# Kernel tuning notes

Measured on AMD Instinct MI355X. Metric: run time of the kernel, lower is better.

Reference implementation:

```python
import jax, jax.numpy as jnp
import numpy as np

D_MODEL = 2048
N_Q = 16
N_KV = 4
HEAD_DIM = 128
WINDOW = 512
ROPE_BASE = 10000.0


def _rope_cos_sin(T, dtype):
    half = HEAD_DIM // 2
    inv_freq = 1.0 / (ROPE_BASE ** (jnp.arange(0, half, dtype=jnp.float32) * 2.0 / HEAD_DIM))
    pos = jnp.arange(T, dtype=jnp.float32)
    ang = pos[:, None] * inv_freq[None, :]            # [T, half]
    emb = jnp.concatenate([ang, ang], axis=-1)        # [T, HEAD_DIM]
    return jnp.cos(emb).astype(dtype), jnp.sin(emb).astype(dtype)


def _rotate_half(x):
    x1, x2 = jnp.split(x, 2, axis=-1)
    return jnp.concatenate([-x2, x1], axis=-1)


def _apply_rope(t, cos, sin):
    # t: [B, H, T, hd]; cos/sin: [T, hd]
    return t * cos[None, None, :, :] + _rotate_half(t) * sin[None, None, :, :]


def setup_inputs() -> dict:
    key = jax.random.key(0)
    ks = jax.random.split(key, 5)
    s = 0.02
    return {
        "x": jax.random.normal(ks[0], (2, 2048, D_MODEL), dtype=jnp.float32),
        "wq": jax.random.normal(ks[1], (D_MODEL, N_Q * HEAD_DIM), dtype=jnp.float32) * s,
        "wk": jax.random.normal(ks[2], (D_MODEL, N_KV * HEAD_DIM), dtype=jnp.float32) * s,
        "wv": jax.random.normal(ks[3], (D_MODEL, N_KV * HEAD_DIM), dtype=jnp.float32) * s,
        "wo": jax.random.normal(ks[4], (N_Q * HEAD_DIM, D_MODEL), dtype=jnp.float32) * s,
    }


def reference(x, wq, wk, wv, wo):
    B, T, _ = x.shape
    q = (x @ wq).reshape(B, T, N_Q, HEAD_DIM).transpose(0, 2, 1, 3)    # [B,Hq,T,hd]
    k = (x @ wk).reshape(B, T, N_KV, HEAD_DIM).transpose(0, 2, 1, 3)   # [B,Hkv,T,hd]
    v = (x @ wv).reshape(B, T, N_KV, HEAD_DIM).transpose(0, 2, 1, 3)

    cos, sin = _rope_cos_sin(T, x.dtype)
    q = _apply_rope(q, cos, sin)
    k = _apply_rope(k, cos, sin)

    # GQA: repeat_interleave kv heads to match q heads
    g = N_Q // N_KV
    k = jnp.repeat(k, g, axis=1)
    v = jnp.repeat(v, g, axis=1)

    scale = 1.0 / np.sqrt(HEAD_DIM)
    scores = jnp.einsum("bhqd,bhkd->bhqk", q, k) * scale

    idx = jnp.arange(T)
    diff = idx[:, None] - idx[None, :]
    keep = (diff >= 0) & (diff < WINDOW)               # causal & sliding window
    scores = jnp.where(keep[None, None, :, :], scores, jnp.finfo(scores.dtype).min)
    attn = jax.nn.softmax(scores, axis=-1)

    out = jnp.einsum("bhqk,bhkd->bhqd", attn, v)       # [B,Hq,T,hd]
    out = out.transpose(0, 2, 1, 3).reshape(B, T, N_Q * HEAD_DIM)
    return out @ wo
```

## Files before the change

### kernel.cpp

```cpp
#include <hip/hip_runtime.h>

#define T_SEQ   2048
#define DM      2048
#define N_Q     16
#define N_KV    4
#define HD      128
#define WIN     512
#define NB      2
#define NQKV    3072
#define QK_SCALE 0.08838834764831845f

typedef short bf16x8 __attribute__((ext_vector_type(8)));
typedef float f32x4  __attribute__((ext_vector_type(4)));

__device__ __forceinline__ unsigned short f2bf(float f) {
    union { float f; unsigned u; } v; v.f = f;
    unsigned u = v.u;
    u += 0x7fffu + ((u >> 16) & 1u);
    return (unsigned short)(u >> 16);
}
__device__ __forceinline__ float bf2f(unsigned short h) {
    union { unsigned u; float f; } v; v.u = ((unsigned)h) << 16;
    return v.f;
}

#define GLOAD_LDS16(g, l) __builtin_amdgcn_global_load_lds( \
    (const __attribute__((address_space(1))) void*)(g),     \
    (__attribute__((address_space(3))) void*)(l), 16, 0, 0)


struct us4 { unsigned short a, b, c, d; };

__global__ __launch_bounds__(256)
void f32_to_bf16_vec(const float* __restrict__ in, unsigned short* __restrict__ out, long n) {
    long i = ((long)blockIdx.x * 256 + threadIdx.x) * 4;
    if (i < n) {
        float4 f = *(const float4*)(in + i);
        us4 o; o.a = f2bf(f.x); o.b = f2bf(f.y); o.c = f2bf(f.z); o.d = f2bf(f.w);
        *(us4*)(out + i) = o;
    }
}

__global__ __launch_bounds__(256)
void transpose_w(const float* __restrict__ in, unsigned short* __restrict__ out, int R, int C) {
    __shared__ float tile[32][33];
    const int c0 = blockIdx.x * 32, r0 = blockIdx.y * 32;
    const int tx = threadIdx.x, ty = threadIdx.y;
#pragma unroll
    for (int i = 0; i < 4; ++i)
        tile[ty + i * 8][tx] = in[(long)(r0 + ty + i * 8) * C + c0 + tx];
    __syncthreads();
#pragma unroll
    for (int i = 0; i < 4; ++i)
        out[(long)(c0 + ty + i * 8) * R + r0 + tx] = f2bf(tile[tx][ty + i * 8]);
}

__global__ __launch_bounds__(256)
void rope_table(float* __restrict__ cosT, float* __restrict__ sinT) {
    const int idx = blockIdx.x * 256 + threadIdx.x;
    const int t = idx >> 6, d = idx & 63;
    const float inv = __expf(-(float)d * (9.210340371976184f / 64.0f));
    const float ang = (float)t * inv;
    cosT[idx] = cosf(ang);
    sinT[idx] = sinf(ang);
}

__global__ __launch_bounds__(256)
void rope_apply(unsigned short* __restrict__ qkv,
                const float* __restrict__ cosT, const float* __restrict__ sinT) {
    const int idx = blockIdx.x * 256 + threadIdx.x;
    const int d = idx & 63;
    const int hh = (idx >> 6) % 20;
    const int row = idx / (64 * 20);
    const int t = row & (T_SEQ - 1);
    const int col = (hh < N_Q) ? hh * HD + d : DM + (hh - N_Q) * HD + d;
    unsigned short* p = qkv + (long)row * NQKV + col;
    const float a = bf2f(p[0]), b = bf2f(p[64]);
    const float c = cosT[t * 64 + d], s = sinT[t * 64 + d];
    float o1 = a * c - b * s;
    float o2 = b * c + a * s;
    if (hh < N_Q) { o1 *= QK_SCALE; o2 *= QK_SCALE; }
    p[0]  = f2bf(o1);
    p[64] = f2bf(o2);
}

__global__ __launch_bounds__(256)
void transpose_v(const unsigned short* __restrict__ qkv, unsigned short* __restrict__ vt) {
    __shared__ unsigned short tile[32][33];
    const int bh = blockIdx.z;
    const int d0 = blockIdx.y * 32;
    const int t0 = blockIdx.x * 32;
    const int tx = threadIdx.x, ty = threadIdx.y;
    const long inbase = (long)(bh >> 2) * T_SEQ;
    const int coff = DM + N_KV * HD + (bh & 3) * HD;
#pragma unroll
    for (int i = 0; i < 4; ++i)
        tile[ty + i * 8][tx] = qkv[(inbase + t0 + ty + i * 8) * NQKV + coff + d0 + tx];
    __syncthreads();
#pragma unroll
    for (int i = 0; i < 4; ++i)
        vt[((long)bh * HD + d0 + ty + i * 8) * T_SEQ + t0 + tx] = tile[tx][ty + i * 8];
}


template<int OUT_BF16>
__global__ __launch_bounds__(256)
void gemm_bt(const unsigned short* __restrict__ A,
             const unsigned short* __restrict__ Bt,
             void* __restrict__ Cvoid, int K, int ldc) {
    __shared__ __align__(16) unsigned short sA[128 * 64];
    __shared__ __align__(16) unsigned short sB[128 * 64];
    const int tid = threadIdx.x;
    const int lane = tid & 63;
    const int wid = tid >> 6;
    const int wr = (wid >> 1) * 64, wc = (wid & 1) * 64;
    const long Arow0 = (long)blockIdx.y * 128;
    const long Brow0 = (long)blockIdx.x * 128;

    f32x4 acc[4][4] = {};

    for (int kt = 0; kt < K; kt += 64) {
        __syncthreads();
#pragma unroll
        for (int n = 0; n < 4; ++n) {
            const int linb = n * 256 + wid * 64;
            const int lin  = linb + lane;
            const int row  = lin >> 3;
            const int sc   = (lin & 7) ^ (row & 7);
            const unsigned short* gA = A  + (Arow0 + row) * K + kt + sc * 8;
            const unsigned short* gB = Bt + (Brow0 + row) * K + kt + sc * 8;
            GLOAD_LDS16(gA, &sA[linb * 8]);
            GLOAD_LDS16(gB, &sB[linb * 8]);
        }
        __syncthreads();
#pragma unroll
        for (int kk = 0; kk < 2; ++kk) {
            bf16x8 av[4], bv[4];
#pragma unroll
            for (int i = 0; i < 4; ++i) {
                const int row = wr + i * 16 + (lane & 15);
                const int c = (kk * 4 + (lane >> 4)) ^ (row & 7);
                av[i] = *(const bf16x8*)&sA[row * 64 + c * 8];
            }
#pragma unroll
            for (int j = 0; j < 4; ++j) {
                const int row = wc + j * 16 + (lane & 15);
                const int c = (kk * 4 + (lane >> 4)) ^ (row & 7);
                bv[j] = *(const bf16x8*)&sB[row * 64 + c * 8];
            }
#pragma unroll
            for (int i = 0; i < 4; ++i)
#pragma unroll
                for (int j = 0; j < 4; ++j)
                    acc[i][j] = __builtin_amdgcn_mfma_f32_16x16x32_bf16(av[i], bv[j], acc[i][j], 0, 0, 0);
        }
    }

    const int r0 = (int)Arow0 + wr + ((lane >> 4) << 2);
    const int c0 = (int)Brow0 + wc + (lane & 15);
    if (OUT_BF16) {
        unsigned short* C = (unsigned short*)Cvoid;
#pragma unroll
        for (int i = 0; i < 4; ++i)
#pragma unroll
            for (int j = 0; j < 4; ++j)
#pragma unroll
                for (int r = 0; r < 4; ++r)
                    C[(long)(r0 + i * 16 + r) * ldc + c0 + j * 16] = f2bf(acc[i][j][r]);
    } else {
        float* C = (float*)Cvoid;
#pragma unroll
        for (int i = 0; i < 4; ++i)
#pragma unroll
            for (int j = 0; j < 4; ++j)
#pragma unroll
                for (int r = 0; r < 4; ++r)
                    C[(long)(r0 + i * 16 + r) * ldc + c0 + j * 16] = acc[i][j][r];
    }
}


__global__ __launch_bounds__(256)
void attn_kernel(const unsigned short* __restrict__ qkv,
                 const unsigned short* __restrict__ vt,
                 unsigned short* __restrict__ aout) {
    const int qt = blockIdx.x, h = blockIdx.y, b = blockIdx.z;
    const int tid = threadIdx.x, lane = tid & 63, w = tid >> 6;
    const int q0w = qt * 64 + w * 16;
    const int hkv = h >> 2;
    const int lo = lane & 15, hi = lane >> 4;

    __shared__ __align__(16) unsigned short sK[64 * 128];
    __shared__ __align__(16) unsigned short sV[128 * 64];
    __shared__ __align__(16) unsigned short plds[4][16 * 64];
    unsigned short* pl = plds[w];

    bf16x8 qf[4];
    {
        const unsigned short* qp = qkv + (long)(b * T_SEQ + q0w + lo) * NQKV + h * HD + hi * 8;
#pragma unroll
        for (int s = 0; s < 4; ++s) qf[s] = *(const bf16x8*)(qp + s * 32);
    }

    f32x4 of[8] = {};
    float m_r[4] = { -1e30f, -1e30f, -1e30f, -1e30f };
    float s_r[4] = { 0.f, 0.f, 0.f, 0.f };

    int kstart = qt * 64 - (WIN - 1);
    if (kstart < 0) kstart = 0;
    kstart &= ~63;
    const int kend = qt * 64 + 63;

    const unsigned short* kbase = qkv + (long)b * T_SEQ * NQKV + DM + hkv * HD;
    const unsigned short* vbase = vt + (long)(b * N_KV + hkv) * HD * T_SEQ;

    int krow[4], kck[4], vrow[4], vck[4];
#pragma unroll
    for (int u = 0; u < 4; ++u) {
        const int i = w * 4 + u;
        krow[u] = i * 4 + (lane >> 4);
        kck[u]  = (lane & 15) ^ (krow[u] & 7);
        vrow[u] = i * 8 + (lane >> 3);
        vck[u]  = (lane & 7) ^ (vrow[u] & 7);
    }

    for (int kt = kstart; kt <= kend; kt += 64) {
        __syncthreads();
#pragma unroll
        for (int u = 0; u < 4; ++u) {
            const int i = w * 4 + u;
            GLOAD_LDS16(kbase + (long)(kt + krow[u]) * NQKV + kck[u] * 8, &sK[i * 512]);
            GLOAD_LDS16(vbase + (long)vrow[u] * T_SEQ + kt + vck[u] * 8, &sV[i * 512]);
        }
        __syncthreads();

        f32x4 sf[4] = {};
        __builtin_amdgcn_s_setprio(1);
#pragma unroll
        for (int n = 0; n < 4; ++n) {
            const int row = n * 16 + lo;
#pragma unroll
            for (int s = 0; s < 4; ++s) {
                const int c = (s * 4 + hi) ^ (row & 7);
                bf16x8 kf = *(const bf16x8*)&sK[row * 128 + c * 8];
                sf[n] = __builtin_amdgcn_mfma_f32_16x16x32_bf16(qf[s], kf, sf[n], 0, 0, 0);
            }
        }
        __builtin_amdgcn_s_setprio(0);

        float pf[4][4];
#pragma unroll
        for (int r = 0; r < 4; ++r) {
            const int q = q0w + hi * 4 + r;
            float sv[4];
#pragma unroll
            for (int n = 0; n < 4; ++n) {
                const int d = q - (kt + n * 16 + lo);
                sv[n] = (d >= 0 && d < WIN) ? sf[n][r] : -1e30f;
            }
            float mx = fmaxf(fmaxf(sv[0], sv[1]), fmaxf(sv[2], sv[3]));
#pragma unroll
            for (int off = 1; off < 16; off <<= 1) mx = fmaxf(mx, __shfl_xor(mx, off));
            const float mnew = fmaxf(m_r[r], mx);
            const float resc = __expf(m_r[r] - mnew);
            float ps = 0.f;
#pragma unroll
            for (int n = 0; n < 4; ++n) { pf[n][r] = __expf(sv[n] - mnew); ps += pf[n][r]; }
#pragma unroll
            for (int off = 1; off < 16; off <<= 1) ps += __shfl_xor(ps, off);
            s_r[r] = s_r[r] * resc + ps;
            m_r[r] = mnew;
#pragma unroll
            for (int j = 0; j < 8; ++j) of[j][r] *= resc;
        }

#pragma unroll
        for (int n = 0; n < 4; ++n)
#pragma unroll
            for (int r = 0; r < 4; ++r) {
                const int row = hi * 4 + r;
                const int key = n * 16 + lo;
                const int sw = ((key >> 3) ^ (row & 7)) * 8 + (key & 7);
                pl[row * 64 + sw] = f2bf(pf[n][r]);
            }
        asm volatile("s_waitcnt lgkmcnt(0)" ::: "memory");
        __builtin_amdgcn_sched_barrier(0);
        bf16x8 pa[2];
#pragma unroll
        for (int ks = 0; ks < 2; ++ks) {
            const int c = (ks * 4 + hi) ^ (lo & 7);
            pa[ks] = *(const bf16x8*)&pl[lo * 64 + c * 8];
        }

        __builtin_amdgcn_s_setprio(1);
#pragma unroll
        for (int j = 0; j < 8; ++j) {
            const int row = j * 16 + lo;
#pragma unroll
            for (int ks = 0; ks < 2; ++ks) {
                const int c = (ks * 4 + hi) ^ (row & 7);
                bf16x8 vf = *(const bf16x8*)&sV[row * 64 + c * 8];
                of[j] = __builtin_amdgcn_mfma_f32_16x16x32_bf16(pa[ks], vf, of[j], 0, 0, 0);
            }
        }
        __builtin_amdgcn_s_setprio(0);
    }

#pragma unroll
    for (int r = 0; r < 4; ++r) {
        const int q = q0w + hi * 4 + r;
        const float inv = 1.0f / s_r[r];
        unsigned short* op = aout + (long)(b * T_SEQ + q) * DM + h * HD + lo;
#pragma unroll
        for (int j = 0; j < 8; ++j) op[j * 16] = f2bf(of[j][r] * inv);
    }
}


extern "C" void kernel_launch(void* const* d_in, const int* in_sizes, int n_in,
                              void* d_out, int out_size, void* d_ws, size_t ws_size,
                              hipStream_t stream) {
    (void)in_sizes; (void)n_in; (void)out_size; (void)ws_size;
    const float* x  = (const float*)d_in[0];
    const float* wq = (const float*)d_in[1];
    const float* wk = (const float*)d_in[2];
    const float* wv = (const float*)d_in[3];
    const float* wo = (const float*)d_in[4];
    float* out = (float*)d_out;
    char* ws = (char*)d_ws;

    unsigned short* xbf   = (unsigned short*)(ws);
    unsigned short* wqkvT = (unsigned short*)(ws + 16777216);
    unsigned short* woT   = (unsigned short*)(ws + 29360128);
    unsigned short* qkv   = (unsigned short*)(ws + 37748736);
    unsigned short* vt    = (unsigned short*)(ws + 62914560);
    unsigned short* aout  = (unsigned short*)(ws + 67108864);
    float* cosT = (float*)(ws + 83886080);
    float* sinT = (float*)(ws + 84410368);

    const long Mx = (long)NB * T_SEQ * DM;
    f32_to_bf16_vec<<<dim3(8192), dim3(256), 0, stream>>>(x, xbf, Mx);
    transpose_w<<<dim3(64, 64), dim3(32, 8), 0, stream>>>(wq, wqkvT, DM, DM);
    transpose_w<<<dim3(16, 64), dim3(32, 8), 0, stream>>>(wk, wqkvT + (long)DM * DM, DM, 512);
    transpose_w<<<dim3(16, 64), dim3(32, 8), 0, stream>>>(wv, wqkvT + (long)(DM + 512) * DM, DM, 512);
    transpose_w<<<dim3(64, 64), dim3(32, 8), 0, stream>>>(wo, woT, DM, DM);
    rope_table<<<dim3(512), dim3(256), 0, stream>>>(cosT, sinT);

    gemm_bt<1><<<dim3(NQKV / 128, 32), dim3(256), 0, stream>>>(xbf, wqkvT, qkv, DM, NQKV);
    rope_apply<<<dim3(20480), dim3(256), 0, stream>>>(qkv, cosT, sinT);
    transpose_v<<<dim3(64, 4, 8), dim3(32, 8), 0, stream>>>(qkv, vt);
    attn_kernel<<<dim3(32, 16, 2), dim3(256), 0, stream>>>(qkv, vt, aout);
    gemm_bt<0><<<dim3(DM / 128, 32), dim3(256), 0, stream>>>(aout, woT, out, DM, DM);
}
```

Measured before the change: 198.6 us.

## Double-buffer attention K/V tiles, transpose score MFMA, lazy softmax rescale, swizzle GEMM grid

The attention kernel now double-buffers K and V tiles in LDS, prefetching the next tile while computing the current one. It swaps the MFMA operands so each lane holds one query row, which cuts the row-max and sum reductions to two shuffles. It folds log2(e) into the Q scale so exp2 can be used, and skips the output rescale unless the max grows by more than 8. The GEMM also remaps block indices across 8 groups for better cache locality, and P is packed to bf16 with a single instruction. In exchange the kernel uses twice the LDS for K/V, which may lower occupancy.

```diff
diff --git a/kernel.cpp b/kernel.cpp
--- a/kernel.cpp
+++ b/kernel.cpp
@@ -8,7 +8,7 @@
 #define WIN     512
 #define NB      2
 #define NQKV    3072
-#define QK_SCALE 0.08838834764831845f
+#define QK_SCALE_L2E 0.12751744f
 
 typedef short bf16x8 __attribute__((ext_vector_type(8)));
 typedef float f32x4  __attribute__((ext_vector_type(4)));
@@ -22,6 +22,11 @@
 __device__ __forceinline__ float bf2f(unsigned short h) {
     union { unsigned u; float f; } v; v.u = ((unsigned)h) << 16;
     return v.f;
+}
+__device__ __forceinline__ unsigned cvt_pk_bf16(float a, float b) {
+    unsigned r;
+    asm("v_cvt_pk_bf16_f32 %0, %1, %2" : "=v"(r) : "v"(a), "v"(b));
+    return r;
 }
 
 #define GLOAD_LDS16(g, l) __builtin_amdgcn_global_load_lds( \
@@ -79,7 +84,7 @@
     const float c = cosT[t * 64 + d], s = sinT[t * 64 + d];
     float o1 = a * c - b * s;
     float o2 = b * c + a * s;
-    if (hh < N_Q) { o1 *= QK_SCALE; o2 *= QK_SCALE; }
+    if (hh < N_Q) { o1 *= QK_SCALE_L2E; o2 *= QK_SCALE_L2E; }
     p[0]  = f2bf(o1);
     p[64] = f2bf(o2);
 }
@@ -114,8 +119,13 @@
     const int lane = tid & 63;
     const int wid = tid >> 6;
     const int wr = (wid >> 1) * 64, wc = (wid & 1) * 64;
-    const long Arow0 = (long)blockIdx.y * 128;
-    const long Brow0 = (long)blockIdx.x * 128;
+
+    const int gx = gridDim.x;
+    const int nwg = gx * gridDim.y;
+    int flat = blockIdx.y * gx + blockIdx.x;
+    flat = (flat & 7) * (nwg >> 3) + (flat >> 3);
+    const long Arow0 = (long)(flat / gx) * 128;
+    const long Brow0 = (long)(flat % gx) * 128;
 
     f32x4 acc[4][4] = {};
 
@@ -190,8 +200,8 @@
     const int hkv = h >> 2;
     const int lo = lane & 15, hi = lane >> 4;
 
-    __shared__ __align__(16) unsigned short sK[64 * 128];
-    __shared__ __align__(16) unsigned short sV[128 * 64];
+    __shared__ __align__(16) unsigned short sK[2][64 * 128];
+    __shared__ __align__(16) unsigned short sV[2][128 * 64];
     __shared__ __align__(16) unsigned short plds[4][16 * 64];
     unsigned short* pl = plds[w];
 
@@ -203,8 +213,8 @@
     }
 
     f32x4 of[8] = {};
-    float m_r[4] = { -1e30f, -1e30f, -1e30f, -1e30f };
-    float s_r[4] = { 0.f, 0.f, 0.f, 0.f };
+    float m_r = -1e30f;
+    float s_r = 0.f;
 
     int kstart = qt * 64 - (WIN - 1);
     if (kstart < 0) kstart = 0;
@@ -224,15 +234,21 @@
         vck[u]  = (lane & 7) ^ (vrow[u] & 7);
     }
 
+#define STAGE(bf, kt_) do {                                                          \
+    _Pragma("unroll")                                                                \
+    for (int u = 0; u < 4; ++u) {                                                    \
+        const int i = w * 4 + u;                                                     \
+        GLOAD_LDS16(kbase + (long)((kt_) + krow[u]) * NQKV + kck[u] * 8, &sK[bf][i * 512]); \
+        GLOAD_LDS16(vbase + (long)vrow[u] * T_SEQ + (kt_) + vck[u] * 8, &sV[bf][i * 512]);  \
+    } } while (0)
+
+    STAGE(0, kstart);
+    asm volatile("s_waitcnt vmcnt(0)" ::: "memory");
+    __syncthreads();
+
+    int buf = 0;
     for (int kt = kstart; kt <= kend; kt += 64) {
-        __syncthreads();
-#pragma unroll
-        for (int u = 0; u < 4; ++u) {
-            const int i = w * 4 + u;
-            GLOAD_LDS16(kbase + (long)(kt + krow[u]) * NQKV + kck[u] * 8, &sK[i * 512]);
-            GLOAD_LDS16(vbase + (long)vrow[u] * T_SEQ + kt + vck[u] * 8, &sV[i * 512]);
-        }
-        __syncthreads();
+        if (kt + 64 <= kend) STAGE(buf ^ 1, kt + 64);
 
         f32x4 sf[4] = {};
         __builtin_amdgcn_s_setprio(1);
@@ -242,47 +258,61 @@
 #pragma unroll
             for (int s = 0; s < 4; ++s) {
                 const int c = (s * 4 + hi) ^ (row & 7);
-                bf16x8 kf = *(const bf16x8*)&sK[row * 128 + c * 8];
-                sf[n] = __builtin_amdgcn_mfma_f32_16x16x32_bf16(qf[s], kf, sf[n], 0, 0, 0);
+                bf16x8 kf = *(const bf16x8*)&sK[buf][row * 128 + c * 8];
+                sf[n] = __builtin_amdgcn_mfma_f32_16x16x32_bf16(kf, qf[s], sf[n], 0, 0, 0);
             }
         }
         __builtin_amdgcn_s_setprio(0);
 
-        float pf[4][4];
-#pragma unroll
-        for (int r = 0; r < 4; ++r) {
-            const int q = q0w + hi * 4 + r;
-            float sv[4];
-#pragma unroll
-            for (int n = 0; n < 4; ++n) {
-                const int d = q - (kt + n * 16 + lo);
-                sv[n] = (d >= 0 && d < WIN) ? sf[n][r] : -1e30f;
-            }
-            float mx = fmaxf(fmaxf(sv[0], sv[1]), fmaxf(sv[2], sv[3]));
-#pragma unroll
-            for (int off = 1; off < 16; off <<= 1) mx = fmaxf(mx, __shfl_xor(mx, off));
-            const float mnew = fmaxf(m_r[r], mx);
-            const float resc = __expf(m_r[r] - mnew);
-            float ps = 0.f;
-#pragma unroll
-            for (int n = 0; n < 4; ++n) { pf[n][r] = __expf(sv[n] - mnew); ps += pf[n][r]; }
-#pragma unroll
-            for (int off = 1; off < 16; off <<= 1) ps += __shfl_xor(ps, off);
-            s_r[r] = s_r[r] * resc + ps;
-            m_r[r] = mnew;
-#pragma unroll
-            for (int j = 0; j < 8; ++j) of[j][r] *= resc;
-        }
-
+        const int q = q0w + lo;
+        float sv[4][4];
+        float mx = -1e30f;
 #pragma unroll
         for (int n = 0; n < 4; ++n)
 #pragma unroll
             for (int r = 0; r < 4; ++r) {
-                const int row = hi * 4 + r;
-                const int key = n * 16 + lo;
-                const int sw = ((key >> 3) ^ (row & 7)) * 8 + (key & 7);
-                pl[row * 64 + sw] = f2bf(pf[n][r]);
-            }
+                const int d = q - (kt + n * 16 + hi * 4 + r);
+                sv[n][r] = (d >= 0 && d < WIN) ? sf[n][r] : -1e30f;
+                mx = fmaxf(mx, sv[n][r]);
+            }
+        mx = fmaxf(mx, __shfl_xor(mx, 16));
+        mx = fmaxf(mx, __shfl_xor(mx, 32));
+
+        if (!__all(mx <= m_r + 8.0f)) {
+            const float mnew = fmaxf(m_r, mx);
+            const float resc = exp2f(m_r - mnew);
+            s_r *= resc;
+            m_r = mnew;
+            float r4[4];
+#pragma unroll
+            for (int r = 0; r < 4; ++r) r4[r] = __shfl(resc, hi * 4 + r);
+#pragma unroll
+            for (int j = 0; j < 8; ++j) {
+                of[j][0] *= r4[0]; of[j][1] *= r4[1];
+                of[j][2] *= r4[2]; of[j][3] *= r4[3];
+            }
+        }
+
+        float pv[4][4];
+        float psum = 0.f;
+#pragma unroll
+        for (int n = 0; n < 4; ++n)
+#pragma unroll
+            for (int r = 0; r < 4; ++r) {
+                pv[n][r] = exp2f(sv[n][r] - m_r);
+                psum += pv[n][r];
+            }
+        psum += __shfl_xor(psum, 16);
+        psum += __shfl_xor(psum, 32);
+        s_r += psum;
+
+        const int swz = (lo & 7) << 3;
+#pragma unroll
+        for (int n = 0; n < 4; ++n) {
+            const int k0 = n * 16 + hi * 4;
+            *(unsigned*)&pl[lo * 64 + (k0 ^ swz)]       = cvt_pk_bf16(pv[n][0], pv[n][1]);
+            *(unsigned*)&pl[lo * 64 + ((k0 + 2) ^ swz)] = cvt_pk_bf16(pv[n][2], pv[n][3]);
+        }
         asm volatile("s_waitcnt lgkmcnt(0)" ::: "memory");
         __builtin_amdgcn_sched_barrier(0);
         bf16x8 pa[2];
@@ -299,18 +329,26 @@
 #pragma unroll
             for (int ks = 0; ks < 2; ++ks) {
                 const int c = (ks * 4 + hi) ^ (row & 7);
-                bf16x8 vf = *(const bf16x8*)&sV[row * 64 + c * 8];
+                bf16x8 vf = *(const bf16x8*)&sV[buf][row * 64 + c * 8];
                 of[j] = __builtin_amdgcn_mfma_f32_16x16x32_bf16(pa[ks], vf, of[j], 0, 0, 0);
             }
         }
         __builtin_amdgcn_s_setprio(0);
-    }
-
+
+        asm volatile("s_waitcnt vmcnt(0)" ::: "memory");
+        __syncthreads();
+        buf ^= 1;
+    }
+#undef STAGE
+
+    float s4[4];
+#pragma unroll
+    for (int r = 0; r < 4; ++r) s4[r] = __shfl(s_r, hi * 4 + r);
 #pragma unroll
     for (int r = 0; r < 4; ++r) {
-        const int q = q0w + hi * 4 + r;
-        const float inv = 1.0f / s_r[r];
-        unsigned short* op = aout + (long)(b * T_SEQ + q) * DM + h * HD + lo;
+        const int qrow = q0w + hi * 4 + r;
+        const float inv = 1.0f / s4[r];
+        unsigned short* op = aout + (long)(b * T_SEQ + qrow) * DM + h * HD + lo;
 #pragma unroll
         for (int j = 0; j < 8; ++j) op[j * 16] = f2bf(of[j][r] * inv);
     }
```

Result: faster. 191.2 us (-3.7%).
